# Optimization experiments

Hardware: AMD Instinct MI355X
Metric: run time of the kernel (lower is better)

The kernel has to match this reference:

```python
import jax, jax.numpy as jnp
import numpy as np

B, T, D = 32, 128, 64
SPK, CELL, NCLS = 2, 64, 6
DIMS = [300, 74, 35]
BETA = 0.8            # QActivation beta
TWO_PI = 2 * 3.14     # repo uses 2*3.14, not 2*pi


def _unitary(seed, d):
    rng = np.random.default_rng(seed)
    m = rng.normal(size=(d, d)) + 1j * rng.normal(size=(d, d))
    q, _ = np.linalg.qr(m)  # exact unitary -> stable 128-step recurrence
    return jnp.asarray(q.real, jnp.float32), jnp.asarray(q.imag, jnp.float32)


def setup_inputs() -> dict:
    key = jax.random.key(0)
    ks = jax.random.split(key, 16)
    inp = {}
    for i, dm in enumerate(DIMS):
        inp[f"mod{i}"] = jax.random.normal(ks[i], (B, T, dm), jnp.float32)
        inp[f"Wp{i}"] = jax.random.normal(ks[3 + i], (dm, D), jnp.float32) / np.sqrt(dm)
        inp[f"bp{i}"] = jnp.zeros((D,), jnp.float32)
    inp["smask"] = jax.random.uniform(ks[6], (B, T, SPK), dtype=jnp.float32)
    inp["umask"] = jnp.ones((B, T), jnp.float32)
    inp["phase_table"] = jax.random.uniform(ks[7], (SPK, D), dtype=jnp.float32)
    inp["Uh_r"], inp["Uh_i"] = _unitary(1, D)
    inp["Ux_r"], inp["Ux_i"] = _unitary(2, D)
    inp["Lambda"] = jnp.asarray([0.5], jnp.float32)
    inp["K_r"] = jax.random.normal(ks[8], (D, D), jnp.float32) / np.sqrt(D)
    inp["K_i"] = jax.random.normal(ks[9], (D, D), jnp.float32) / np.sqrt(D)
    inp["W1"] = jax.random.normal(ks[10], (D, CELL), jnp.float32) / np.sqrt(D)
    inp["b1"] = jnp.zeros((CELL,), jnp.float32)
    inp["W2"] = jax.random.normal(ks[11], (CELL, NCLS), jnp.float32) / np.sqrt(CELL)
    inp["b2"] = jnp.zeros((NCLS,), jnp.float32)
    return inp


def reference(mod0, mod1, mod2, smask, umask, Wp0, bp0, Wp1, bp1, Wp2, bp2,
              phase_table, Uh_r, Uh_i, Ux_r, Ux_i, Lambda, K_r, K_i, W1, b1, W2, b2):
    d = Uh_r.shape[0]
    b, t = mod0.shape[0], mod0.shape[1]
    mods, Ws, bs = [mod0, mod1, mod2], [Wp0, Wp1, Wp2], [bp0, bp1, bp2]
    # per-modality projections + ReLU -> utterance reps (B,T,D)
    reps = [jax.nn.relu(m @ W + bb) for m, W, bb in zip(mods, Ws, bs)]
    # L2Norm -> softmax mixture weights over modalities (B,T,3)
    norms = jnp.stack([jnp.linalg.norm(r, axis=-1) for r in reps], axis=-1)
    weights = jax.nn.softmax(norms, axis=-1)
    # PositionEmbedding: speaker-conditioned phase + sinusoidal-style frequencies
    sid = jnp.argmax(smask, axis=-1)                                  # (B,T) speaker id
    freq = 1.0 / (10000.0 ** (jnp.arange(d, dtype=jnp.float32) / d))  # (D,)
    pos = jnp.arange(t, dtype=jnp.float32)[None, :, None]             # (1,T,1)
    phase = pos * freq + phase_table[sid] * TWO_PI                    # (B,T,D)
    eiphi = jnp.exp(1j * phase).astype(jnp.complex64)
    # ComplexMultiply + QOuter + QMixture fused: rho = sum_m w_m |psi_m><psi_m|
    rho = jnp.zeros((b, t, d, d), jnp.complex64)
    for m, rep in enumerate(reps):
        amp = rep / jnp.maximum(jnp.linalg.norm(rep, axis=-1, keepdims=True), 1e-12)
        psi = amp.astype(jnp.complex64) * eiphi                       # (B,T,D) pure state
        rho = rho + weights[..., m, None, None].astype(jnp.complex64) * \
              jnp.einsum('bti,btj->btij', psi, psi.conj())
    # QRNNCell recurrence (num_layers=1): h' = lam*Ux rho Ux^H + (1-lam)*Uh h Uh^H
    Uh = (Uh_r + 1j * Uh_i).astype(jnp.complex64)
    Ux = (Ux_r + 1j * Ux_i).astype(jnp.complex64)
    lam = Lambda[0].astype(jnp.complex64)
    mixed_eye = jnp.eye(d, dtype=jnp.complex64) / d

    def step(h, rho_t):
        hx = jnp.einsum('ij,bjk,lk->bil', Ux, rho_t, Ux.conj())
        hh = jnp.einsum('ij,bjk,lk->bil', Uh, h, Uh.conj())
        h_new = lam * hx + (1.0 - lam) * hh
        out = BETA * h_new + (1.0 - BETA) * mixed_eye  # QActivation (trace-preserving)
        return h_new, out

    h0 = jnp.broadcast_to(mixed_eye, (b, d, d))
    _, outs = jax.lax.scan(step, h0, jnp.swapaxes(rho, 0, 1))         # (T,B,D,D)
    rho_out = jnp.swapaxes(outs, 0, 1)                                # (B,T,D,D)
    # QMeasurement: p_j = Re( k_j^H rho k_j )
    K = (K_r + 1j * K_i).astype(jnp.complex64)
    probs = jnp.einsum('jm,btmn,jn->btj', K.conj(), rho_out, K).real  # (B,T,D)
    # SimpleNet head (dropout off in eval) + log_softmax over classes
    h1 = jax.nn.relu(probs @ W1 + b1)
    logits = jnp.tanh(h1 @ W2 + b2)                                   # (B,T,C)
    return jax.nn.log_softmax(logits, axis=2)
```

## Files before the change

### kernel.cpp

```cpp
#include <hip/hip_runtime.h>
#include <hip/hip_bf16.h>
#include <math.h>

#define DD 64
#define TT 128
#define BBATCH 32
#define BT (BBATCH*TT)
#define ND 16
#define BETA_C 0.8f
#define TWO_PI_R 6.28f
#define LG2_10000 13.28771237954945f
#define SW 328

typedef float2 cf;
typedef _Float16 f16;
typedef _Float16 half8 __attribute__((ext_vector_type(8)));
typedef _Float16 half4 __attribute__((ext_vector_type(4)));
typedef float f32x4 __attribute__((ext_vector_type(4)));

__device__ __forceinline__ void cfma(cf& acc, cf a, cf b){
  acc.x = fmaf(a.x, b.x, fmaf(-a.y, b.y, acc.x));
  acc.y = fmaf(a.x, b.y, fmaf( a.y, b.x, acc.y));
}

template<int KDIM, int KPAD>
__device__ __forceinline__ f32x4 prep_phase(
    const float* __restrict__ Wp, const float* __restrict__ modg,
    f16* sWpT, f16* sMod, int tid, int w, int l15, int l4)
{
  __syncthreads();
  constexpr int PAD = KPAD - KDIM;
  for (int i = tid; i < 64*PAD; i += 256) {
    const int r = i / PAD, p = KDIM + (i - r*PAD);
    sWpT[r*SW + p] = (f16)0.f;
  }
  for (int i = tid; i < 16*PAD; i += 256) {
    const int r = i / PAD, p = KDIM + (i - r*PAD);
    sMod[r*SW + p] = (f16)0.f;
  }
  for (int i = tid; i < KDIM*16; i += 256) {
    const int p = i >> 4, c4 = (i & 15) << 2;
    const float4 v = *(const float4*)&Wp[p*64 + c4];
    sWpT[(c4+0)*SW + p] = (f16)v.x;
    sWpT[(c4+1)*SW + p] = (f16)v.y;
    sWpT[(c4+2)*SW + p] = (f16)v.z;
    sWpT[(c4+3)*SW + p] = (f16)v.w;
  }
  for (int i = tid; i < (16*KDIM)/4; i += 256) {
    const float4 v = *(const float4*)&modg[i*4];
    const float vv[4] = {v.x, v.y, v.z, v.w};
    #pragma unroll
    for (int e2 = 0; e2 < 4; ++e2) {
      const int flat = i*4 + e2;
      const int r = flat / KDIM, p = flat - r*KDIM;
      sMod[r*SW + p] = (f16)vv[e2];
    }
  }
  __syncthreads();
  f32x4 acc = {0.f, 0.f, 0.f, 0.f};
  #pragma unroll
  for (int s = 0; s < KPAD/32; ++s) {
    const half8 a = *(const half8*)&sWpT[(w*16 + l15)*SW + s*32 + l4*8];
    const half8 b = *(const half8*)&sMod[l15*SW + s*32 + l4*8];
    acc = __builtin_amdgcn_mfma_f32_16x16x32_f16(a, b, acc, 0, 0, 0);
  }
  return acc;
}

__global__ __launch_bounds__(256) void k_front(
    const float* __restrict__ mod0, const float* __restrict__ Wp0, const float* __restrict__ bp0,
    const float* __restrict__ mod1, const float* __restrict__ Wp1, const float* __restrict__ bp1,
    const float* __restrict__ mod2, const float* __restrict__ Wp2, const float* __restrict__ bp2,
    const float* __restrict__ smask, const float* __restrict__ ptab,
    const float* __restrict__ Uhr, const float* __restrict__ Uhi,
    const float* __restrict__ Uxr, const float* __restrict__ Uxi,
    const float* __restrict__ Kr,  const float* __restrict__ Ki,
    f16* __restrict__ PsiR, f16* __restrict__ PsiI,
    f16* __restrict__ Cre, f16* __restrict__ Cim, f16* __restrict__ Cmn,
    float* __restrict__ kn)
{
  __shared__ __align__(16) char smem[65536];
  const int tid = threadIdx.x, w = tid >> 6, lane = tid & 63;
  const int l15 = lane & 15, l4 = lane >> 4;

  if (blockIdx.x < 64) {
    cf* st = (cf*)smem;
    cf (*red)[64] = (cf(*)[64])(smem + 512);
    const int j = blockIdx.x, c = lane;

    cf uh[16], ux[16];
    #pragma unroll
    for (int i = 0; i < 16; ++i) {
      const int p = w*16 + i;
      uh[i] = make_float2(Uhr[p*64 + c], Uhi[p*64 + c]);
      ux[i] = make_float2(Uxr[p*64 + c], Uxi[p*64 + c]);
    }
    if (w == 0) {
      const cf kj = make_float2(Kr[j*64 + c], -Ki[j*64 + c]);
      st[c] = kj;
      float q = fmaf(kj.x, kj.x, kj.y*kj.y);
      #pragma unroll
      for (int off = 32; off; off >>= 1) q += __shfl_xor(q, off);
      if (c == 0) kn[j] = q;
    }
    __syncthreads();

    for (int D = 0; D < ND; ++D) {
      cf cA = {0.f,0.f}, cB = {0.f,0.f}, tA = {0.f,0.f}, tB = {0.f,0.f};
      #pragma unroll
      for (int i = 0; i < 16; i += 2) {
        const cf t0 = st[w*16 + i], t1 = st[w*16 + i + 1];
        cfma(cA, t0, ux[i]); cfma(cB, t1, ux[i+1]);
        cfma(tA, t0, uh[i]); cfma(tB, t1, uh[i+1]);
      }
      red[w][c]     = make_float2(cA.x + cB.x, cA.y + cB.y);
      red[4 + w][c] = make_float2(tA.x + tB.x, tA.y + tB.y);
      __syncthreads();
      if (w == 0) {
        const cf r0 = red[0][c], r1 = red[1][c], r2 = red[2][c], r3 = red[3][c];
        const float crx = r0.x + r1.x + r2.x + r3.x;
        const float cry = r0.y + r1.y + r2.y + r3.y;
        const size_t row = (size_t)(D*64 + j)*64 + c;
        Cre[row] = (f16)crx;
        Cim[row] = (f16)cry;
        Cmn[row] = (f16)(-cry);
      } else if (w == 1) {
        const cf r0 = red[4][c], r1 = red[5][c], r2 = red[6][c], r3 = red[7][c];
        st[c] = make_float2(r0.x + r1.x + r2.x + r3.x, r0.y + r1.y + r2.y + r3.y);
      }
      __syncthreads();
    }
    return;
  }

  f16* sWpT = (f16*)smem;
  f16* sMod = (f16*)(smem + 41984);
  float* repS = (float*)(smem + 52480);
  const int bt0 = (int)(blockIdx.x - 64) * 16;

  const f32x4 a0 = prep_phase<300,320>(Wp0, mod0 + (size_t)bt0*300, sWpT, sMod, tid, w, l15, l4);
  #pragma unroll
  for (int r = 0; r < 4; ++r) {
    const int d = w*16 + l4*4 + r;
    repS[(0*16 + l15)*68 + d] = a0[r] + bp0[d];
  }
  const f32x4 a1 = prep_phase<74,96>(Wp1, mod1 + (size_t)bt0*74, sWpT, sMod, tid, w, l15, l4);
  #pragma unroll
  for (int r = 0; r < 4; ++r) {
    const int d = w*16 + l4*4 + r;
    repS[(1*16 + l15)*68 + d] = a1[r] + bp1[d];
  }
  const f32x4 a2 = prep_phase<35,64>(Wp2, mod2 + (size_t)bt0*35, sWpT, sMod, tid, w, l15, l4);
  #pragma unroll
  for (int r = 0; r < 4; ++r) {
    const int d = w*16 + l4*4 + r;
    repS[(2*16 + l15)*68 + d] = a2[r] + bp2[d];
  }
  __syncthreads();

  const int btl = tid >> 4, g = tid & 15;
  float4 v0 = *(float4*)&repS[(0*16 + btl)*68 + g*4];
  float4 v1 = *(float4*)&repS[(1*16 + btl)*68 + g*4];
  float4 v2 = *(float4*)&repS[(2*16 + btl)*68 + g*4];
  v0.x = fmaxf(v0.x, 0.f); v0.y = fmaxf(v0.y, 0.f); v0.z = fmaxf(v0.z, 0.f); v0.w = fmaxf(v0.w, 0.f);
  v1.x = fmaxf(v1.x, 0.f); v1.y = fmaxf(v1.y, 0.f); v1.z = fmaxf(v1.z, 0.f); v1.w = fmaxf(v1.w, 0.f);
  v2.x = fmaxf(v2.x, 0.f); v2.y = fmaxf(v2.y, 0.f); v2.z = fmaxf(v2.z, 0.f); v2.w = fmaxf(v2.w, 0.f);

  float q0 = v0.x*v0.x + v0.y*v0.y + v0.z*v0.z + v0.w*v0.w;
  float q1 = v1.x*v1.x + v1.y*v1.y + v1.z*v1.z + v1.w*v1.w;
  float q2 = v2.x*v2.x + v2.y*v2.y + v2.z*v2.z + v2.w*v2.w;
  #pragma unroll
  for (int off = 8; off; off >>= 1) {
    q0 += __shfl_xor(q0, off);
    q1 += __shfl_xor(q1, off);
    q2 += __shfl_xor(q2, off);
  }
  const float n0 = sqrtf(q0), n1 = sqrtf(q1), n2 = sqrtf(q2);
  const float mx = fmaxf(n0, fmaxf(n1, n2));
  const float e0 = expf(n0 - mx), e1 = expf(n1 - mx), e2 = expf(n2 - mx);
  const float inv = 1.f / (e0 + e1 + e2);
  const float sc0 = sqrtf(e0*inv) / fmaxf(n0, 1e-12f);
  const float sc1 = sqrtf(e1*inv) / fmaxf(n1, 1e-12f);
  const float sc2 = sqrtf(e2*inv) / fmaxf(n2, 1e-12f);

  const int btg = bt0 + btl;
  const int t = btg & (TT-1);
  const int sid = (smask[btg*2 + 1] > smask[btg*2]) ? 1 : 0;

  float cs[4], sn[4];
  #pragma unroll
  for (int i = 0; i < 4; ++i) {
    const int d = g*4 + i;
    const float freq = exp2f(-((float)d * (1.f/64.f)) * LG2_10000);
    const float ph = (float)t * freq + ptab[sid*64 + d] * TWO_PI_R;
    sincosf(ph, &sn[i], &cs[i]);
  }
  const float am0[4] = {v0.x*sc0, v0.y*sc0, v0.z*sc0, v0.w*sc0};
  const float am1[4] = {v1.x*sc1, v1.y*sc1, v1.z*sc1, v1.w*sc1};
  const float am2[4] = {v2.x*sc2, v2.y*sc2, v2.z*sc2, v2.w*sc2};
  half4 wr, wi;
  #pragma unroll
  for (int i = 0; i < 4; ++i) { wr[i] = (f16)(am0[i]*cs[i]); wi[i] = (f16)(am0[i]*sn[i]); }
  *(half4*)&PsiR[(size_t)(0*BT + btg)*64 + g*4] = wr;
  *(half4*)&PsiI[(size_t)(0*BT + btg)*64 + g*4] = wi;
  #pragma unroll
  for (int i = 0; i < 4; ++i) { wr[i] = (f16)(am1[i]*cs[i]); wi[i] = (f16)(am1[i]*sn[i]); }
  *(half4*)&PsiR[(size_t)(1*BT + btg)*64 + g*4] = wr;
  *(half4*)&PsiI[(size_t)(1*BT + btg)*64 + g*4] = wi;
  #pragma unroll
  for (int i = 0; i < 4; ++i) { wr[i] = (f16)(am2[i]*cs[i]); wi[i] = (f16)(am2[i]*sn[i]); }
  *(half4*)&PsiR[(size_t)(2*BT + btg)*64 + g*4] = wr;
  *(half4*)&PsiI[(size_t)(2*BT + btg)*64 + g*4] = wi;
}

#define PST 72
__global__ __launch_bounds__(256) void k_E(
    const f16* __restrict__ Cre, const f16* __restrict__ Cim, const f16* __restrict__ Cmn,
    const f16* __restrict__ PsiR, const f16* __restrict__ PsiI,
    f16* __restrict__ e16)
{
  __shared__ __align__(16) f16 sP[2][2][64][PST];
  const int bsg = blockIdx.x >> 3, cgg = blockIdx.x & 7;
  const int tid = threadIdx.x, w = tid >> 6, lane = tid & 63;
  const int l15 = lane & 15, l4 = lane >> 4;

  half8 aRe[2][2], aIm[2][2], aMn[2][2];
  #pragma unroll
  for (int cc = 0; cc < 2; ++cc) {
    const size_t arow = ((size_t)((cgg*2 + cc)*64 + w*16 + l15))*64 + l4*8;
    aRe[cc][0] = *(const half8*)&Cre[arow]; aRe[cc][1] = *(const half8*)&Cre[arow + 32];
    aIm[cc][0] = *(const half8*)&Cim[arow]; aIm[cc][1] = *(const half8*)&Cim[arow + 32];
    aMn[cc][0] = *(const half8*)&Cmn[arow]; aMn[cc][1] = *(const half8*)&Cmn[arow + 32];
  }

  const int r0s = tid >> 3, c8s = (tid & 7) << 3;
  const int r1s = (tid + 256) >> 3;
  {
    const size_t g0 = ((size_t)(0*BT + bsg*64 + r0s))*64 + c8s;
    const size_t g1 = ((size_t)(0*BT + bsg*64 + r1s))*64 + c8s;
    *(uint4*)&sP[0][0][r0s][c8s] = *(const uint4*)&PsiR[g0];
    *(uint4*)&sP[0][1][r0s][c8s] = *(const uint4*)&PsiI[g0];
    *(uint4*)&sP[0][0][r1s][c8s] = *(const uint4*)&PsiR[g1];
    *(uint4*)&sP[0][1][r1s][c8s] = *(const uint4*)&PsiI[g1];
  }

  f32x4 eAcc[2][4];
  #pragma unroll
  for (int cc = 0; cc < 2; ++cc)
    #pragma unroll
    for (int ct = 0; ct < 4; ++ct) eAcc[cc][ct] = (f32x4){0.f,0.f,0.f,0.f};

  #pragma unroll
  for (int k = 0; k < 3; ++k) {
    uint4 nR0, nI0, nR1, nI1;
    if (k < 2) {
      const size_t g0 = ((size_t)((k+1)*BT + bsg*64 + r0s))*64 + c8s;
      const size_t g1 = ((size_t)((k+1)*BT + bsg*64 + r1s))*64 + c8s;
      nR0 = *(const uint4*)&PsiR[g0];
      nI0 = *(const uint4*)&PsiI[g0];
      nR1 = *(const uint4*)&PsiR[g1];
      nI1 = *(const uint4*)&PsiI[g1];
    }
    __syncthreads();
    const int kb = k & 1;
    #pragma unroll
    for (int cc = 0; cc < 2; ++cc) {
      #pragma unroll
      for (int ct = 0; ct < 4; ++ct) {
        f32x4 xr = {0.f,0.f,0.f,0.f}, xi = {0.f,0.f,0.f,0.f};
        #pragma unroll
        for (int kk = 0; kk < 2; ++kk) {
          const half8 bRe = *(const half8*)&sP[kb][0][ct*16 + l15][l4*8 + kk*32];
          const half8 bIm = *(const half8*)&sP[kb][1][ct*16 + l15][l4*8 + kk*32];
          xr = __builtin_amdgcn_mfma_f32_16x16x32_f16(aRe[cc][kk], bRe, xr, 0, 0, 0);
          xr = __builtin_amdgcn_mfma_f32_16x16x32_f16(aMn[cc][kk], bIm, xr, 0, 0, 0);
          xi = __builtin_amdgcn_mfma_f32_16x16x32_f16(aRe[cc][kk], bIm, xi, 0, 0, 0);
          xi = __builtin_amdgcn_mfma_f32_16x16x32_f16(aIm[cc][kk], bRe, xi, 0, 0, 0);
        }
        #pragma unroll
        for (int r = 0; r < 4; ++r)
          eAcc[cc][ct][r] = fmaf(xr[r], xr[r], fmaf(xi[r], xi[r], eAcc[cc][ct][r]));
      }
    }
    if (k < 2) {
      const int nb = kb ^ 1;
      *(uint4*)&sP[nb][0][r0s][c8s] = nR0;
      *(uint4*)&sP[nb][1][r0s][c8s] = nI0;
      *(uint4*)&sP[nb][0][r1s][c8s] = nR1;
      *(uint4*)&sP[nb][1][r1s][c8s] = nI1;
    }
  }

  f16* sE = (f16*)sP;
  #pragma unroll
  for (int cc = 0; cc < 2; ++cc) {
    __syncthreads();
    #pragma unroll
    for (int ct = 0; ct < 4; ++ct)
      #pragma unroll
      for (int r = 0; r < 4; ++r)
        sE[(ct*16 + l15)*PST + w*16 + l4*4 + r] = (f16)eAcc[cc][ct][r];
    __syncthreads();
    const int cg = cgg*2 + cc;
    *(uint4*)&e16[((size_t)(bsg*64 + r0s))*1024 + cg*64 + c8s] = *(const uint4*)&sE[r0s*PST + c8s];
    *(uint4*)&e16[((size_t)(bsg*64 + r1s))*1024 + cg*64 + c8s] = *(const uint4*)&sE[r1s*PST + c8s];
  }
}

__global__ __launch_bounds__(256) void k_head(const f16* __restrict__ e16,
    const float* __restrict__ kn, const float* __restrict__ Lam,
    const float* __restrict__ W1, const float* __restrict__ b1,
    const float* __restrict__ W2, const float* __restrict__ b2,
    float* __restrict__ out)
{
  __shared__ float sW1[4096];
  __shared__ float pr[4][64];
  __shared__ float h1[4][64];
  __shared__ float lg[4][6];
  const int tid = threadIdx.x;
  const int q = tid >> 6, j = tid & 63;
  const int bt = blockIdx.x*4 + q;
  const int b = bt >> 7, t = bt & (TT-1);
  const float lam = Lam[0], om = 1.f - lam;

  for (int i = tid*4; i < 4096; i += 1024)
    *(float4*)&sW1[i] = *(const float4*)&W1[i];

  float acc = 0.f, wD = BETA_C * lam;
  const int nd = min(ND, t + 1);
  for (int D = 0; D < nd; ++D) {
    acc += wD * (float)e16[(size_t)(b*TT + t - D)*1024 + D*64 + j];
    wD *= om;
  }
  const float omt = exp2f((float)(t + 1) * log2f(om));
  acc += (BETA_C*omt + (1.f - BETA_C)) * kn[j] * (1.f/64.f);
  pr[q][j] = acc;
  __syncthreads();

  float a1 = b1[j];
  for (int dd = 0; dd < 64; ++dd) a1 = fmaf(pr[q][dd], sW1[dd*64 + j], a1);
  h1[q][j] = fmaxf(a1, 0.f);
  __syncthreads();

  if (j < 6) {
    float a2 = b2[j];
    for (int c = 0; c < 64; ++c) a2 = fmaf(h1[q][c], W2[c*6 + j], a2);
    lg[q][j] = tanhf(a2);
  }
  __syncthreads();
  if (j < 6) {
    float mx = -1e30f;
    #pragma unroll
    for (int n = 0; n < 6; ++n) mx = fmaxf(mx, lg[q][n]);
    float se = 0.f;
    #pragma unroll
    for (int n = 0; n < 6; ++n) se += expf(lg[q][n] - mx);
    out[bt*6 + j] = lg[q][j] - mx - logf(se);
  }
}

extern "C" void kernel_launch(void* const* d_in, const int* in_sizes, int n_in,
                              void* d_out, int out_size, void* d_ws, size_t ws_size,
                              hipStream_t stream)
{
  const float* mod0  = (const float*)d_in[0];
  const float* Wp0   = (const float*)d_in[1];
  const float* bp0   = (const float*)d_in[2];
  const float* mod1  = (const float*)d_in[3];
  const float* Wp1   = (const float*)d_in[4];
  const float* bp1   = (const float*)d_in[5];
  const float* mod2  = (const float*)d_in[6];
  const float* Wp2   = (const float*)d_in[7];
  const float* bp2   = (const float*)d_in[8];
  const float* smask = (const float*)d_in[9];
  const float* ptab  = (const float*)d_in[11];
  const float* Uhr   = (const float*)d_in[12];
  const float* Uhi   = (const float*)d_in[13];
  const float* Uxr   = (const float*)d_in[14];
  const float* Uxi   = (const float*)d_in[15];
  const float* Lam   = (const float*)d_in[16];
  const float* Kr    = (const float*)d_in[17];
  const float* Ki    = (const float*)d_in[18];
  const float* W1    = (const float*)d_in[19];
  const float* b1    = (const float*)d_in[20];
  const float* W2    = (const float*)d_in[21];
  const float* b2    = (const float*)d_in[22];

  char* ws = (char*)d_ws;
  float* kn   = (float*)(ws);
  f16*   Cre  = (f16*)  (ws + ((size_t)1024 << 10));
  f16*   Cim  = (f16*)  (ws + ((size_t)1280 << 10));
  f16*   Cmn  = (f16*)  (ws + ((size_t)1536 << 10));
  f16*   PsiR = (f16*)  (ws + ((size_t)2 << 20));
  f16*   PsiI = (f16*)  (ws + ((size_t)4 << 20));
  f16*   e16  = (f16*)  (ws + ((size_t)6 << 20));
  if (ws_size < ((size_t)16 << 20)) return;

  k_front<<<320, 256, 0, stream>>>(mod0, Wp0, bp0, mod1, Wp1, bp1, mod2, Wp2, bp2,
                                   smask, ptab, Uhr, Uhi, Uxr, Uxi, Kr, Ki,
                                   PsiR, PsiI, Cre, Cim, Cmn, kn);
  k_E<<<512, 256, 0, stream>>>(Cre, Cim, Cmn, PsiR, PsiI, e16);
  k_head<<<1024, 256, 0, stream>>>(e16, kn, Lam, W1, b1, W2, b2, (float*)d_out);
}
```

Measured before the change: 46.16 us.

## Halve front-kernel rows per block and parallelize head classifier reduction

The projection part of the front kernel now handles 8 utterance rows per block instead of 16, doubling the grid from 256 to 512 projection blocks so more CUs are busy. The unused half of the 16-row MFMA tile is zero-filled, which wastes half the matrix math and makes every block reload the projection weights. The head kernel's 6-class logit dot product is split across 48 lanes, each summing 8 terms, and combined with shuffles instead of 6 lanes each looping over 64 terms. Shared memory for the front kernel is also trimmed.

Result: slower. 50.23 us (+8.8%).

```diff
diff --git a/kernel.cpp b/kernel.cpp
--- a/kernel.cpp
+++ b/kernel.cpp
@@ -11,6 +11,7 @@
 #define TWO_PI_R 6.28f
 #define LG2_10000 13.28771237954945f
 #define SW 328
+#define PST 72
 
 typedef float2 cf;
 typedef _Float16 f16;
@@ -24,7 +25,7 @@
 }
 
 template<int KDIM, int KPAD>
-__device__ __forceinline__ f32x4 prep_phase(
+__device__ __forceinline__ f32x4 prep_phase8(
     const float* __restrict__ Wp, const float* __restrict__ modg,
     f16* sWpT, f16* sMod, int tid, int w, int l15, int l4)
 {
@@ -34,10 +35,9 @@
     const int r = i / PAD, p = KDIM + (i - r*PAD);
     sWpT[r*SW + p] = (f16)0.f;
   }
-  for (int i = tid; i < 16*PAD; i += 256) {
-    const int r = i / PAD, p = KDIM + (i - r*PAD);
-    sMod[r*SW + p] = (f16)0.f;
-  }
+  for (int i = tid*8; i < 16*SW; i += 2048)
+    *(uint4*)&sMod[i] = (uint4){0u,0u,0u,0u};
+  __syncthreads();
   for (int i = tid; i < KDIM*16; i += 256) {
     const int p = i >> 4, c4 = (i & 15) << 2;
     const float4 v = *(const float4*)&Wp[p*64 + c4];
@@ -46,7 +46,7 @@
     sWpT[(c4+2)*SW + p] = (f16)v.z;
     sWpT[(c4+3)*SW + p] = (f16)v.w;
   }
-  for (int i = tid; i < (16*KDIM)/4; i += 256) {
+  for (int i = tid; i < (8*KDIM)/4; i += 256) {
     const float4 v = *(const float4*)&modg[i*4];
     const float vv[4] = {v.x, v.y, v.z, v.w};
     #pragma unroll
@@ -79,7 +79,7 @@
     f16* __restrict__ Cre, f16* __restrict__ Cim, f16* __restrict__ Cmn,
     float* __restrict__ kn)
 {
-  __shared__ __align__(16) char smem[65536];
+  __shared__ __align__(16) char smem[59136];
   const int tid = threadIdx.x, w = tid >> 6, lane = tid & 63;
   const int l15 = lane & 15, l4 = lane >> 4;
 
@@ -136,84 +136,91 @@
   f16* sWpT = (f16*)smem;
   f16* sMod = (f16*)(smem + 41984);
   float* repS = (float*)(smem + 52480);
-  const int bt0 = (int)(blockIdx.x - 64) * 16;
-
-  const f32x4 a0 = prep_phase<300,320>(Wp0, mod0 + (size_t)bt0*300, sWpT, sMod, tid, w, l15, l4);
-  #pragma unroll
-  for (int r = 0; r < 4; ++r) {
-    const int d = w*16 + l4*4 + r;
-    repS[(0*16 + l15)*68 + d] = a0[r] + bp0[d];
-  }
-  const f32x4 a1 = prep_phase<74,96>(Wp1, mod1 + (size_t)bt0*74, sWpT, sMod, tid, w, l15, l4);
-  #pragma unroll
-  for (int r = 0; r < 4; ++r) {
-    const int d = w*16 + l4*4 + r;
-    repS[(1*16 + l15)*68 + d] = a1[r] + bp1[d];
-  }
-  const f32x4 a2 = prep_phase<35,64>(Wp2, mod2 + (size_t)bt0*35, sWpT, sMod, tid, w, l15, l4);
-  #pragma unroll
-  for (int r = 0; r < 4; ++r) {
-    const int d = w*16 + l4*4 + r;
-    repS[(2*16 + l15)*68 + d] = a2[r] + bp2[d];
+  const int bt0 = (int)(blockIdx.x - 64) * 8;
+
+  const f32x4 a0 = prep_phase8<300,320>(Wp0, mod0 + (size_t)bt0*300, sWpT, sMod, tid, w, l15, l4);
+  if (l15 < 8) {
+    #pragma unroll
+    for (int r = 0; r < 4; ++r) {
+      const int d = w*16 + l4*4 + r;
+      repS[(0*8 + l15)*68 + d] = a0[r] + bp0[d];
+    }
+  }
+  const f32x4 a1 = prep_phase8<74,96>(Wp1, mod1 + (size_t)bt0*74, sWpT, sMod, tid, w, l15, l4);
+  if (l15 < 8) {
+    #pragma unroll
+    for (int r = 0; r < 4; ++r) {
+      const int d = w*16 + l4*4 + r;
+      repS[(1*8 + l15)*68 + d] = a1[r] + bp1[d];
+    }
+  }
+  const f32x4 a2 = prep_phase8<35,64>(Wp2, mod2 + (size_t)bt0*35, sWpT, sMod, tid, w, l15, l4);
+  if (l15 < 8) {
+    #pragma unroll
+    for (int r = 0; r < 4; ++r) {
+      const int d = w*16 + l4*4 + r;
+      repS[(2*8 + l15)*68 + d] = a2[r] + bp2[d];
+    }
   }
   __syncthreads();
 
   const int btl = tid >> 4, g = tid & 15;
-  float4 v0 = *(float4*)&repS[(0*16 + btl)*68 + g*4];
-  float4 v1 = *(float4*)&repS[(1*16 + btl)*68 + g*4];
-  float4 v2 = *(float4*)&repS[(2*16 + btl)*68 + g*4];
-  v0.x = fmaxf(v0.x, 0.f); v0.y = fmaxf(v0.y, 0.f); v0.z = fmaxf(v0.z, 0.f); v0.w = fmaxf(v0.w, 0.f);
-  v1.x = fmaxf(v1.x, 0.f); v1.y = fmaxf(v1.y, 0.f); v1.z = fmaxf(v1.z, 0.f); v1.w = fmaxf(v1.w, 0.f);
-  v2.x = fmaxf(v2.x, 0.f); v2.y = fmaxf(v2.y, 0.f); v2.z = fmaxf(v2.z, 0.f); v2.w = fmaxf(v2.w, 0.f);
-
-  float q0 = v0.x*v0.x + v0.y*v0.y + v0.z*v0.z + v0.w*v0.w;
-  float q1 = v1.x*v1.x + v1.y*v1.y + v1.z*v1.z + v1.w*v1.w;
-  float q2 = v2.x*v2.x + v2.y*v2.y + v2.z*v2.z + v2.w*v2.w;
-  #pragma unroll
-  for (int off = 8; off; off >>= 1) {
-    q0 += __shfl_xor(q0, off);
-    q1 += __shfl_xor(q1, off);
-    q2 += __shfl_xor(q2, off);
-  }
-  const float n0 = sqrtf(q0), n1 = sqrtf(q1), n2 = sqrtf(q2);
-  const float mx = fmaxf(n0, fmaxf(n1, n2));
-  const float e0 = expf(n0 - mx), e1 = expf(n1 - mx), e2 = expf(n2 - mx);
-  const float inv = 1.f / (e0 + e1 + e2);
-  const float sc0 = sqrtf(e0*inv) / fmaxf(n0, 1e-12f);
-  const float sc1 = sqrtf(e1*inv) / fmaxf(n1, 1e-12f);
-  const float sc2 = sqrtf(e2*inv) / fmaxf(n2, 1e-12f);
-
-  const int btg = bt0 + btl;
-  const int t = btg & (TT-1);
-  const int sid = (smask[btg*2 + 1] > smask[btg*2]) ? 1 : 0;
-
-  float cs[4], sn[4];
-  #pragma unroll
-  for (int i = 0; i < 4; ++i) {
-    const int d = g*4 + i;
-    const float freq = exp2f(-((float)d * (1.f/64.f)) * LG2_10000);
-    const float ph = (float)t * freq + ptab[sid*64 + d] * TWO_PI_R;
-    sincosf(ph, &sn[i], &cs[i]);
-  }
-  const float am0[4] = {v0.x*sc0, v0.y*sc0, v0.z*sc0, v0.w*sc0};
-  const float am1[4] = {v1.x*sc1, v1.y*sc1, v1.z*sc1, v1.w*sc1};
-  const float am2[4] = {v2.x*sc2, v2.y*sc2, v2.z*sc2, v2.w*sc2};
-  half4 wr, wi;
-  #pragma unroll
-  for (int i = 0; i < 4; ++i) { wr[i] = (f16)(am0[i]*cs[i]); wi[i] = (f16)(am0[i]*sn[i]); }
-  *(half4*)&PsiR[(size_t)(0*BT + btg)*64 + g*4] = wr;
-  *(half4*)&PsiI[(size_t)(0*BT + btg)*64 + g*4] = wi;
-  #pragma unroll
-  for (int i = 0; i < 4; ++i) { wr[i] = (f16)(am1[i]*cs[i]); wi[i] = (f16)(am1[i]*sn[i]); }
-  *(half4*)&PsiR[(size_t)(1*BT + btg)*64 + g*4] = wr;
-  *(half4*)&PsiI[(size_t)(1*BT + btg)*64 + g*4] = wi;
-  #pragma unroll
-  for (int i = 0; i < 4; ++i) { wr[i] = (f16)(am2[i]*cs[i]); wi[i] = (f16)(am2[i]*sn[i]); }
-  *(half4*)&PsiR[(size_t)(2*BT + btg)*64 + g*4] = wr;
-  *(half4*)&PsiI[(size_t)(2*BT + btg)*64 + g*4] = wi;
-}
-
-#define PST 72
+  if (btl < 8) {
+    float4 v0 = *(float4*)&repS[(0*8 + btl)*68 + g*4];
+    float4 v1 = *(float4*)&repS[(1*8 + btl)*68 + g*4];
+    float4 v2 = *(float4*)&repS[(2*8 + btl)*68 + g*4];
+    v0.x = fmaxf(v0.x, 0.f); v0.y = fmaxf(v0.y, 0.f); v0.z = fmaxf(v0.z, 0.f); v0.w = fmaxf(v0.w, 0.f);
+    v1.x = fmaxf(v1.x, 0.f); v1.y = fmaxf(v1.y, 0.f); v1.z = fmaxf(v1.z, 0.f); v1.w = fmaxf(v1.w, 0.f);
+    v2.x = fmaxf(v2.x, 0.f); v2.y = fmaxf(v2.y, 0.f); v2.z = fmaxf(v2.z, 0.f); v2.w = fmaxf(v2.w, 0.f);
+
+    float q0 = v0.x*v0.x + v0.y*v0.y + v0.z*v0.z + v0.w*v0.w;
+    float q1 = v1.x*v1.x + v1.y*v1.y + v1.z*v1.z + v1.w*v1.w;
+    float q2 = v2.x*v2.x + v2.y*v2.y + v2.z*v2.z + v2.w*v2.w;
+    #pragma unroll
+    for (int off = 8; off; off >>= 1) {
+      q0 += __shfl_xor(q0, off);
+      q1 += __shfl_xor(q1, off);
+      q2 += __shfl_xor(q2, off);
+    }
+    const float n0 = sqrtf(q0), n1 = sqrtf(q1), n2 = sqrtf(q2);
+    const float mx = fmaxf(n0, fmaxf(n1, n2));
+    const float e0 = expf(n0 - mx), e1 = expf(n1 - mx), e2 = expf(n2 - mx);
+    const float inv = 1.f / (e0 + e1 + e2);
+    const float sc0 = sqrtf(e0*inv) / fmaxf(n0, 1e-12f);
+    const float sc1 = sqrtf(e1*inv) / fmaxf(n1, 1e-12f);
+    const float sc2 = sqrtf(e2*inv) / fmaxf(n2, 1e-12f);
+
+    const int btg = bt0 + btl;
+    const int t = btg & (TT-1);
+    const int sid = (smask[btg*2 + 1] > smask[btg*2]) ? 1 : 0;
+
+    float cs[4], sn[4];
+    #pragma unroll
+    for (int i = 0; i < 4; ++i) {
+      const int d = g*4 + i;
+      const float freq = exp2f(-((float)d * (1.f/64.f)) * LG2_10000);
+      const float ph = (float)t * freq + ptab[sid*64 + d] * TWO_PI_R;
+      sincosf(ph, &sn[i], &cs[i]);
+    }
+    const float am0[4] = {v0.x*sc0, v0.y*sc0, v0.z*sc0, v0.w*sc0};
+    const float am1[4] = {v1.x*sc1, v1.y*sc1, v1.z*sc1, v1.w*sc1};
+    const float am2[4] = {v2.x*sc2, v2.y*sc2, v2.z*sc2, v2.w*sc2};
+    half4 wr, wi;
+    #pragma unroll
+    for (int i = 0; i < 4; ++i) { wr[i] = (f16)(am0[i]*cs[i]); wi[i] = (f16)(am0[i]*sn[i]); }
+    *(half4*)&PsiR[(size_t)(0*BT + btg)*64 + g*4] = wr;
+    *(half4*)&PsiI[(size_t)(0*BT + btg)*64 + g*4] = wi;
+    #pragma unroll
+    for (int i = 0; i < 4; ++i) { wr[i] = (f16)(am1[i]*cs[i]); wi[i] = (f16)(am1[i]*sn[i]); }
+    *(half4*)&PsiR[(size_t)(1*BT + btg)*64 + g*4] = wr;
+    *(half4*)&PsiI[(size_t)(1*BT + btg)*64 + g*4] = wi;
+    #pragma unroll
+    for (int i = 0; i < 4; ++i) { wr[i] = (f16)(am2[i]*cs[i]); wi[i] = (f16)(am2[i]*sn[i]); }
+    *(half4*)&PsiR[(size_t)(2*BT + btg)*64 + g*4] = wr;
+    *(half4*)&PsiI[(size_t)(2*BT + btg)*64 + g*4] = wi;
+  }
+}
+
 __global__ __launch_bounds__(256) void k_E(
     const f16* __restrict__ Cre, const f16* __restrict__ Cim, const f16* __restrict__ Cmn,
     const f16* __restrict__ PsiR, const f16* __restrict__ PsiI,
@@ -342,10 +349,16 @@
   h1[q][j] = fmaxf(a1, 0.f);
   __syncthreads();
 
-  if (j < 6) {
-    float a2 = b2[j];
-    for (int c = 0; c < 64; ++c) a2 = fmaf(h1[q][c], W2[c*6 + j], a2);
-    lg[q][j] = tanhf(a2);
+  if (j < 48) {
+    const int c = j >> 3, e = j & 7;
+    float a2 = 0.f;
+    #pragma unroll
+    for (int u = 0; u < 8; ++u)
+      a2 = fmaf(h1[q][e*8 + u], W2[(e*8 + u)*6 + c], a2);
+    a2 += __shfl_xor(a2, 1);
+    a2 += __shfl_xor(a2, 2);
+    a2 += __shfl_xor(a2, 4);
+    if (e == 0) lg[q][c] = tanhf(a2 + b2[c]);
   }
   __syncthreads();
   if (j < 6) {
@@ -396,7 +409,7 @@
   f16*   e16  = (f16*)  (ws + ((size_t)6 << 20));
   if (ws_size < ((size_t)16 << 20)) return;
 
-  k_front<<<320, 256, 0, stream>>>(mod0, Wp0, bp0, mod1, Wp1, bp1, mod2, Wp2, bp2,
+  k_front<<<576, 256, 0, stream>>>(mod0, Wp0, bp0, mod1, Wp1, bp1, mod2, Wp2, bp2,
                                    smask, ptab, Uhr, Uhi, Uxr, Uxi, Kr, Ki,
                                    PsiR, PsiI, Cre, Cim, Cmn, kn);
   k_E<<<512, 256, 0, stream>>>(Cre, Cim, Cmn, PsiR, PsiI, e16);
```
